# Kernel optimization log

Hardware: AMD Instinct MI355X
Metric: run time of the kernel (lower is better)

The kernel has to match this reference:

```python
import jax, jax.numpy as jnp
import numpy as np

NB_ATOMS = 128
NB_CH = 1
ATOM = 12          # atom_size
BATCH = 8
HW = 75            # -> 64x64 patch grid
LAM = 0.1          # soft-threshold level of the L1 proximal
UNROLL = 2         # unroll_steps
FISTA_ITERS = 15   # fixed inner FISTA iterations (replaces res-based stop)


def _prox(u):
    # soft-thresholding (prox of lam*||.||_1)
    return jnp.sign(u) * jnp.maximum(jnp.abs(u) - LAM, 0.0)


def _conv(x, w):
    # valid cross-correlation, NCHW / OIHW (== F.conv2d)
    return jax.lax.conv_general_dilated(x, w, (1, 1), 'VALID',
                                        dimension_numbers=('NCHW', 'OIHW', 'NCHW'))


def _fold(patches, H, W):
    # patches: [B, Ph, Pw, a, a] -> overlap-add to [B, 1, H, W] (== F.fold)
    B, Ph, Pw, a, _ = patches.shape
    out = jnp.zeros((B, H, W), patches.dtype)
    for di in range(a):              # fixed small kernel loop (a*a = 144 slots)
        for dj in range(a):
            out = out.at[:, di:di + Ph, dj:dj + Pw].add(patches[:, :, :, di, dj])
    return out[:, None]


def _fista(c0, X, q, mu):
    # standard FISTA on 0.5*||D^T c - y_patch||^2 + lam*||c||_1 with step mu
    def body(i, st):
        c, z, t = st
        cn = _prox(z - (z @ X - q) * mu)
        tn = (1.0 + jnp.sqrt(1.0 + 4.0 * t * t)) / 2.0
        zn = cn + ((t - 1.0) / tn) * (cn - c)
        return (cn, zn, tn)
    c, _, _ = jax.lax.fori_loop(0, FISTA_ITERS, body, (c0, c0, jnp.float32(1.0)))
    return c


def setup_inputs() -> dict:
    key = jax.random.key(0)
    k1, k2 = jax.random.split(key)
    y = jax.random.normal(k1, (BATCH, NB_CH, HW, HW), dtype=jnp.float32)
    atoms = jax.random.normal(k2, (NB_ATOMS, NB_CH, ATOM, ATOM), dtype=jnp.float32) / 1500.0
    beta = jnp.float32(0.1)
    mu = jnp.float32(1.0)
    return {"y": y, "atoms": atoms, "beta": beta, "mu": mu}


def reference(y, atoms, beta, mu):
    B, C, H, W = y.shape
    N, a = atoms.shape[0], atoms.shape[-1]
    beta = jax.nn.relu(beta)
    mu = jax.nn.relu(mu)
    # normalize atoms: zero-mean, unit L2 rows, then spectral norm / sqrt(mu)
    A = atoms - atoms.mean(axis=(1, 2, 3), keepdims=True)
    Af = A.reshape(N, -1)
    Af = Af / jnp.linalg.norm(Af, axis=1, keepdims=True)
    Af = Af / (jnp.linalg.norm(Af, ord=2) * jnp.sqrt(mu))
    atoms_n = Af.reshape(N, C, a, a)
    X = Af @ Af.T                                   # [N, N] gram
    Ph, Pw = H - a + 1, W - a + 1
    n_patch = B * Ph * Pw
    mean_filter = jnp.ones((1, 1, a, a), y.dtype) / (a * a)
    patch_mean = _conv(y, mean_filter).reshape(n_patch, 1, 1, 1)
    divisors = _fold(jnp.ones((B, Ph, Pw, a, a), y.dtype), H, W)  # overlap counts
    goal = y
    c = jnp.zeros((n_patch, N), y.dtype)
    sg = jax.lax.stop_gradient
    for _ in range(UNROLL):
        q = _conv(goal, atoms_n).transpose(0, 2, 3, 1).reshape(n_patch, N)
        cf = sg(_fista(sg(c), sg(X), sg(q), sg(mu)))   # torch.no_grad inner solve
        cf = _prox(cf - (cf @ X - q) * mu)             # one differentiable step
        pred = jnp.einsum('pn,ncij->pcij', cf, atoms_n) + patch_mean  # [P,1,a,a]
        pred = _fold(pred.reshape(B, Ph, Pw, a, a), H, W)
        goal = (y + beta * pred) / (1.0 + beta * divisors)
        c = cf
    return goal
```

## Files before the change

kernel.cpp:

```cpp
#include <hip/hip_runtime.h>
#include <stdint.h>

#define AA 144
#define LAM 0.1f

#define OFS_SC    0
#define OFS_AF1   64
#define OFS_G     36928
#define OFS_S0    53312
#define OFS_S1    69696
#define OFS_X     86080
#define OFS_PM    139328
#define OFS_GOAL  172096
#define OFS_CF    4411456
#define OFS_PRED  8605760
#define OFS_ATB   OFS_S0
#define OFS_ANTB  OFS_S1


typedef __attribute__((ext_vector_type(8))) short short8_t;
typedef __attribute__((ext_vector_type(4))) float f32x4;
typedef __attribute__((ext_vector_type(2))) float f32x2;

__device__ __forceinline__ unsigned short f2bf(float f) {
    union { float f; uint32_t u; } x; x.f = f;
    uint32_t u = x.u;
    return (unsigned short)((u + 0x7FFFu + ((u >> 16) & 1u)) >> 16);
}
__device__ __forceinline__ float bf2f(unsigned short u) {
    union { float f; uint32_t i; } x; x.i = ((uint32_t)u) << 16; return x.f;
}
__device__ __forceinline__ uint32_t pack_bf(float a, float b) {
    union { float f; uint32_t u; } xa, xb; xa.f = a; xb.f = b;
    return __builtin_amdgcn_perm(xb.u + 0x8000u, xa.u + 0x8000u, 0x07060302u);
}

#define PSTR 136
__global__ __launch_bounds__(1024) void k_setup(const float* atoms, const float* mu_p,
                                                float* ws, const float* y) {
    __shared__ unsigned short ABf[128 * 168];
    __shared__ unsigned short Pb[2][128 * PSTR];
    __shared__ float tr_arr[10];
    __shared__ float v[128];
    __shared__ float red[256];
    int t = threadIdx.x;
    if (blockIdx.x != 0) {
        int e = (blockIdx.x - 1) * 1024 + t;
        if (e < 45000) ws[OFS_GOAL + e] = y[e];
        if (e < 32768) {
            int b = e >> 12, pi = (e >> 6) & 63, pj = e & 63;
            const float* yb = y + b * 5625;
            float s = 0.f;
            for (int di = 0; di < 12; ++di) {
                const float* row = yb + (pi + di) * 75 + pj;
                #pragma unroll
                for (int dj = 0; dj < 12; ++dj) s += row[dj];
            }
            ws[OFS_PM + e] = s * (1.0f / 144.0f);
        }
        return;
    }
    int lane = t & 63, w = t >> 6;
    int col = lane & 15, quad = lane >> 4;
    if (t < 10) tr_arr[t] = (t == 0) ? 128.0f : 0.f;

    {
        int a = t >> 3, sub = t & 7;
        const float* ap = atoms + a * AA + sub * 18;
        float s = 0.f;
        #pragma unroll
        for (int k = 0; k < 18; ++k) s += ap[k];
        s += __shfl_xor(s, 1, 8); s += __shfl_xor(s, 2, 8); s += __shfl_xor(s, 4, 8);
        float mean = s * (1.0f / 144.0f);
        float ss = 0.f;
        #pragma unroll
        for (int k = 0; k < 18; ++k) { float d = ap[k] - mean; ss = fmaf(d, d, ss); }
        ss += __shfl_xor(ss, 1, 8); ss += __shfl_xor(ss, 2, 8); ss += __shfl_xor(ss, 4, 8);
        float rn = 1.0f / sqrtf(ss);
        #pragma unroll
        for (int k = 0; k < 18; ++k) {
            float av = (ap[k] - mean) * rn;
            ws[OFS_AF1 + a * AA + sub * 18 + k] = av;
            ABf[a * 168 + sub * 18 + k] = f2bf(av);
        }
        if (sub == 0) {
            #pragma unroll
            for (int k = AA; k < 160; ++k) ABf[a * 168 + k] = 0;
        }
    }
    __syncthreads();

    {
        uint32_t* D32 = (uint32_t*)Pb[0];
        float* G = ws + OFS_G;
        int mt = w & 7, gh = w >> 3;
        short8_t af[5];
        #pragma unroll
        for (int s = 0; s < 5; ++s)
            af[s] = *(const short8_t*)&ABf[(mt * 16 + col) * 168 + s * 32 + quad * 8];
        #pragma unroll
        for (int gi = 0; gi < 2; ++gi) {
            int g = gh * 2 + gi;
            short8_t b0[5], b1[5];
            #pragma unroll
            for (int s = 0; s < 5; ++s) {
                b0[s] = *(const short8_t*)&ABf[((2 * g) * 16 + col) * 168 + s * 32 + quad * 8];
                b1[s] = *(const short8_t*)&ABf[((2 * g + 1) * 16 + col) * 168 + s * 32 + quad * 8];
            }
            f32x4 a0 = (f32x4){0.f, 0.f, 0.f, 0.f};
            f32x4 a1 = (f32x4){0.f, 0.f, 0.f, 0.f};
            #pragma unroll
            for (int s = 0; s < 5; ++s) {
                a0 = __builtin_amdgcn_mfma_f32_16x16x32_bf16(af[s], b0[s], a0, 0, 0, 0);
                a1 = __builtin_amdgcn_mfma_f32_16x16x32_bf16(af[s], b1[s], a1, 0, 0, 0);
            }
            #pragma unroll
            for (int r = 0; r < 4; ++r) {
                int m = mt * 16 + quad * 4 + r;
                G[m * 128 + g * 32 + col] = a0[r];
                G[m * 128 + g * 32 + 16 + col] = a1[r];
                D32[m * 68 + g * 16 + col] = pack_bf(a0[r], a1[r]);
            }
        }
    }
    __syncthreads();

    int cur = 0;
    #pragma unroll 1
    for (int j = 0; j < 8; ++j) {
        float trn = tr_arr[j];
        float inv2 = 1.0f / (trn * trn);
        const unsigned short* S = Pb[cur];
        uint32_t* D32 = (uint32_t*)Pb[cur ^ 1];
        int mt = w & 7, nh = w >> 3;
        short8_t af[4];
        #pragma unroll
        for (int s = 0; s < 4; ++s)
            af[s] = *(const short8_t*)&S[(mt * 16 + col) * PSTR + s * 32 + quad * 8];
        #pragma unroll
        for (int pr = 0; pr < 2; ++pr) {
            int ntE = 4 * nh + 2 * pr, ntO = ntE + 1;
            short8_t bE[4], bO[4];
            #pragma unroll
            for (int s = 0; s < 4; ++s) {
                bE[s] = *(const short8_t*)&S[(ntE * 16 + col) * PSTR + s * 32 + quad * 8];
                bO[s] = *(const short8_t*)&S[(ntO * 16 + col) * PSTR + s * 32 + quad * 8];
            }
            f32x4 aE = (f32x4){0.f, 0.f, 0.f, 0.f};
            f32x4 aO = (f32x4){0.f, 0.f, 0.f, 0.f};
            #pragma unroll
            for (int s = 0; s < 4; ++s) {
                aE = __builtin_amdgcn_mfma_f32_16x16x32_bf16(af[s], bE[s], aE, 0, 0, 0);
                aO = __builtin_amdgcn_mfma_f32_16x16x32_bf16(af[s], bO[s], aO, 0, 0, 0);
            }
            int nE = ntE * 16 + col, nO = ntO * 16 + col;
            #pragma unroll
            for (int r = 0; r < 4; ++r) {
                float x0 = aE[r] * inv2, x1 = aO[r] * inv2;
                int row = mt * 16 + quad * 4 + r;
                D32[row * 68 + (ntE >> 1) * 16 + col] = pack_bf(x0, x1);
                if (row == nE) atomicAdd(&tr_arr[j + 1], x0);
                if (row == nO) atomicAdd(&tr_arr[j + 1], x1);
            }
        }
        __syncthreads();
        cur ^= 1;
    }

    {
        int a = t >> 3, sub = t & 7;
        const unsigned short* S = Pb[cur];
        float s = 0.f;
        #pragma unroll
        for (int k = 0; k < 16; ++k) s += bf2f(S[a * PSTR + sub * 16 + k]);
        s += __shfl_xor(s, 1, 8); s += __shfl_xor(s, 2, 8); s += __shfl_xor(s, 4, 8);
        if (sub == 0) v[a] = s;
    }
    __syncthreads();
    {
        int a = t >> 3, sub = t & 7;
        const float* G = ws + OFS_G;
        float wv = 0.f;
        #pragma unroll
        for (int k = 0; k < 16; ++k)
            wv = fmaf(G[a * 128 + sub * 16 + k], v[sub * 16 + k], wv);
        wv += __shfl_xor(wv, 1, 8); wv += __shfl_xor(wv, 2, 8); wv += __shfl_xor(wv, 4, 8);
        if (sub == 0) { red[a] = v[a] * wv; red[128 + a] = v[a] * v[a]; }
    }
    __syncthreads();
    for (int off = 64; off > 0; off >>= 1) {
        if (t < off) { red[t] += red[t + off]; red[128 + t] += red[128 + t + off]; }
        __syncthreads();
    }
    if (t == 0) {
        float lam = red[0] / red[128];
        float mu = fmaxf(mu_p[0], 0.0f);
        ws[OFS_SC + 16] = 1.0f / (lam * mu);
        ws[OFS_SC + 17] = 1.0f / (sqrtf(lam) * sqrtf(mu));
    }
}

__global__ __launch_bounds__(256) void k_finalize(float* ws) {
    int idx = blockIdx.x * 256 + threadIdx.x;
    float scX = ws[OFS_SC + 16], scA = ws[OFS_SC + 17];
    if (idx < 16384) {
        int n = idx >> 7, ks = idx & 127;
        int g = ks >> 5, rem = ks & 31, u = rem >> 1, v = rem & 1;
        int k = g * 32 + v * 16 + u;
        ((unsigned short*)(ws + OFS_X))[idx] = f2bf(ws[OFS_G + n * 128 + k] * scX);
    } else if (idx < 36864) {
        int e = idx - 16384;
        int n = e / 160, k = e - n * 160;
        float v = (k < 144) ? ws[OFS_AF1 + n * 144 + k] * scA : 0.f;
        ((unsigned short*)(ws + OFS_ATB))[e] = f2bf(v);
    } else {
        int e = idx - 36864;
        int jp = e >> 7, ks = e & 127;
        int g = ks >> 5, rem = ks & 31, u = rem >> 1, v = rem & 1;
        int n = g * 32 + v * 16 + u;
        ((unsigned short*)(ws + OFS_ANTB))[e] = f2bf(ws[OFS_AF1 + n * 144 + jp] * scA);
    }
}

__global__ __launch_bounds__(256) void k_fista(const unsigned short* XPB, const float* goal,
                                               const unsigned short* ATB,
                                               const unsigned short* ANTBP,
                                               const float* pm, float* cfg, float* pred,
                                               const float* mu_p, int first, int write_cf) {
    __shared__ float gls[12 * 44];
    __shared__ unsigned short Atile[32 * 168];
    __shared__ unsigned short Zbuf[2][32 * 136];
    int t = threadIdx.x;
    int lane = t & 63, w = t >> 6;
    int col = lane & 15, quad = lane >> 4;
    int nb = w * 32;
    int blk = blockIdx.x;
    int b = blk >> 7, pi = (blk >> 1) & 63, h = blk & 1;
    int p0 = blk * 32;
    float mu = fmaxf(mu_p[0], 0.0f);
    const f32x2 mu2 = (f32x2){mu, mu};
    const f32x2 lam2 = (f32x2){LAM, LAM};
    const f32x2 nlam2 = (f32x2){-LAM, -LAM};

    for (int e = t; e < 528; e += 256) {
        int r = e / 44, cc = e - r * 44;
        int gc = h * 32 + cc;
        gls[e] = (gc < 75) ? goal[b * 5625 + (pi + r) * 75 + gc] : 0.f;
    }
    __syncthreads();
    {
        uint32_t* A32 = (uint32_t*)Atile;
        #pragma unroll
        for (int i = 0; i < 10; ++i) {
            int pe = t + i * 256;
            int m = pe / 80, q32 = pe - m * 80;
            int kk = q32 * 2;
            float v0 = 0.f, v1 = 0.f;
            if (kk < 144) {
                int di = kk / 12, dj = kk - di * 12;
                v0 = gls[di * 44 + m + dj];
                int k1 = kk + 1, di1 = k1 / 12, dj1 = k1 - di1 * 12;
                v1 = gls[di1 * 44 + m + dj1];
            }
            A32[m * 84 + q32] = pack_bf(v0, v1);
        }
    }
    __syncthreads();

    f32x2 qv2[2][4];
    {
        short8_t bfq[2][5];
        #pragma unroll
        for (int nt = 0; nt < 2; ++nt)
            #pragma unroll
            for (int s = 0; s < 5; ++s)
                bfq[nt][s] = *(const short8_t*)&ATB[(nb + nt * 16 + col) * 160 + s * 32 + quad * 8];
        #pragma unroll
        for (int mt = 0; mt < 2; ++mt) {
            short8_t af[5];
            #pragma unroll
            for (int s = 0; s < 5; ++s)
                af[s] = *(const short8_t*)&Atile[(mt * 16 + col) * 168 + s * 32 + quad * 8];
            f32x4 acc0 = (f32x4){0.f, 0.f, 0.f, 0.f};
            f32x4 acc1 = (f32x4){0.f, 0.f, 0.f, 0.f};
            #pragma unroll
            for (int s = 0; s < 5; ++s) {
                acc0 = __builtin_amdgcn_mfma_f32_16x16x32_bf16(af[s], bfq[0][s], acc0, 0, 0, 0);
                acc1 = __builtin_amdgcn_mfma_f32_16x16x32_bf16(af[s], bfq[1][s], acc1, 0, 0, 0);
            }
            #pragma unroll
            for (int r = 0; r < 4; ++r) qv2[mt][r] = (f32x2){acc0[r], acc1[r]};
        }
    }

    short8_t xf[2][4];
    #pragma unroll
    for (int nt = 0; nt < 2; ++nt)
        #pragma unroll
        for (int s = 0; s < 4; ++s)
            xf[nt][s] = *(const short8_t*)&XPB[(nb + nt * 16 + col) * 128 + s * 32 + quad * 8];

    uint32_t* Z32w = (uint32_t*)Zbuf[0];
    f32x2 cv2[2][4], zo2[2][4];
    #pragma unroll
    for (int mt = 0; mt < 2; ++mt)
        #pragma unroll
        for (int r = 0; r < 4; ++r) {
            int row = mt * 16 + quad * 4 + r;
            int p = p0 + row;
            float c0 = 0.f, c1 = 0.f;
            if (!first) {
                c0 = cfg[p * 128 + nb + col];
                c1 = cfg[p * 128 + nb + 16 + col];
            }
            cv2[mt][r] = (f32x2){c0, c1};
            zo2[mt][r] = (f32x2){c0, c1};
            Z32w[row * 68 + 16 * w + col] = pack_bf(c0, c1);
        }
    __syncthreads();

    f32x4 acc[2][2];
    auto matmul = [&](const unsigned short* Zr) {
        short8_t af[2][4];
        #pragma unroll
        for (int mt = 0; mt < 2; ++mt)
            #pragma unroll
            for (int s = 0; s < 4; ++s)
                af[mt][s] = *(const short8_t*)&Zr[(mt * 16 + col) * 136 + s * 32 + quad * 8];
        #pragma unroll
        for (int mt = 0; mt < 2; ++mt)
            #pragma unroll
            for (int nt = 0; nt < 2; ++nt)
                acc[mt][nt] = (f32x4){0.f, 0.f, 0.f, 0.f};
        #pragma unroll
        for (int s = 0; s < 4; ++s)
            #pragma unroll
            for (int mt = 0; mt < 2; ++mt)
                #pragma unroll
                for (int nt = 0; nt < 2; ++nt)
                    acc[mt][nt] = __builtin_amdgcn_mfma_f32_16x16x32_bf16(
                        af[mt][s], xf[nt][s], acc[mt][nt], 0, 0, 0);
    };

    float tm = 1.0f;
    int cur = 0;
    #pragma unroll 1
    for (int it = 0; it < 14; ++it) {
        matmul(Zbuf[cur]);
        float tnn = 0.5f * (1.0f + sqrtf(1.0f + 4.0f * tm * tm));
        float fm = (tm - 1.0f) / tnn;
        tm = tnn;
        f32x2 fm2 = (f32x2){fm, fm};
        uint32_t* Zw = (uint32_t*)Zbuf[cur ^ 1];
        #pragma unroll
        for (int mt = 0; mt < 2; ++mt)
            #pragma unroll
            for (int r = 0; r < 4; ++r) {
                f32x2 a2 = (f32x2){acc[mt][0][r], acc[mt][1][r]};
                f32x2 u2 = mu2 * (qv2[mt][r] - a2) + zo2[mt][r];
                f32x2 cl2 = __builtin_elementwise_min(
                                __builtin_elementwise_max(u2, nlam2), lam2);
                f32x2 cn2 = u2 - cl2;
                f32x2 zn2 = fm2 * (cn2 - cv2[mt][r]) + cn2;
                cv2[mt][r] = cn2;
                zo2[mt][r] = zn2;
                Zw[(mt * 16 + quad * 4 + r) * 68 + 16 * w + col] = pack_bf(zn2[0], zn2[1]);
            }
        __syncthreads();
        cur ^= 1;
    }
    {
        matmul(Zbuf[cur]);
        uint32_t* Zw = (uint32_t*)Zbuf[cur ^ 1];
        #pragma unroll
        for (int mt = 0; mt < 2; ++mt)
            #pragma unroll
            for (int r = 0; r < 4; ++r) {
                f32x2 a2 = (f32x2){acc[mt][0][r], acc[mt][1][r]};
                f32x2 u2 = mu2 * (qv2[mt][r] - a2) + zo2[mt][r];
                f32x2 cl2 = __builtin_elementwise_min(
                                __builtin_elementwise_max(u2, nlam2), lam2);
                f32x2 cn2 = u2 - cl2;
                cv2[mt][r] = cn2;
                Zw[(mt * 16 + quad * 4 + r) * 68 + 16 * w + col] = pack_bf(cn2[0], cn2[1]);
            }
        __syncthreads();
        cur ^= 1;
    }
    {
        matmul(Zbuf[cur]);
        uint32_t* Zw = (uint32_t*)Zbuf[cur ^ 1];
        #pragma unroll
        for (int mt = 0; mt < 2; ++mt)
            #pragma unroll
            for (int r = 0; r < 4; ++r) {
                int row = mt * 16 + quad * 4 + r;
                f32x2 a2 = (f32x2){acc[mt][0][r], acc[mt][1][r]};
                f32x2 u2 = mu2 * (qv2[mt][r] - a2) + cv2[mt][r];
                f32x2 cl2 = __builtin_elementwise_min(
                                __builtin_elementwise_max(u2, nlam2), lam2);
                f32x2 cf2 = u2 - cl2;
                if (write_cf) {
                    cfg[(p0 + row) * 128 + nb + col] = cf2[0];
                    cfg[(p0 + row) * 128 + nb + 16 + col] = cf2[1];
                }
                Zw[row * 68 + 16 * w + col] = pack_bf(cf2[0], cf2[1]);
            }
        __syncthreads();
        cur ^= 1;
    }

    {
        int jt0 = (w == 0) ? 0 : (2 * w + 1);
        int jtn = (w == 0) ? 3 : 2;
        const unsigned short* Zr = Zbuf[cur];
        short8_t af[2][4];
        #pragma unroll
        for (int mt = 0; mt < 2; ++mt)
            #pragma unroll
            for (int s = 0; s < 4; ++s)
                af[mt][s] = *(const short8_t*)&Zr[(mt * 16 + col) * 136 + s * 32 + quad * 8];
        f32x4 accp[2][3];
        #pragma unroll
        for (int mt = 0; mt < 2; ++mt)
            #pragma unroll
            for (int ji = 0; ji < 3; ++ji)
                accp[mt][ji] = (f32x4){0.f, 0.f, 0.f, 0.f};
        #pragma unroll
        for (int ji = 0; ji < 3; ++ji) {
            if (ji < jtn) {
                int jt = jt0 + ji;
                short8_t bf4[4];
                #pragma unroll
                for (int s = 0; s < 4; ++s)
                    bf4[s] = *(const short8_t*)&ANTBP[(jt * 16 + col) * 128 + s * 32 + quad * 8];
                #pragma unroll
                for (int mt = 0; mt < 2; ++mt)
                    #pragma unroll
                    for (int s = 0; s < 4; ++s)
                        accp[mt][ji] = __builtin_amdgcn_mfma_f32_16x16x32_bf16(
                            af[mt][s], bf4[s], accp[mt][ji], 0, 0, 0);
            }
        }
        #pragma unroll
        for (int mt = 0; mt < 2; ++mt)
            #pragma unroll
            for (int r = 0; r < 4; ++r) {
                int p = p0 + mt * 16 + quad * 4 + r;
                float pmv = pm[p];
                #pragma unroll
                for (int ji = 0; ji < 3; ++ji)
                    if (ji < jtn)
                        pred[p * 144 + (jt0 + ji) * 16 + col] = accp[mt][ji][r] + pmv;
            }
    }
}

__global__ __launch_bounds__(256) void k_fold(const float* y, const float* beta_p,
                                              const float* pred, float* goal,
                                              float* out, int write_out) {
    __shared__ float P[12 * 832];
    int i = blockIdx.x, b = blockIdx.y;
    int t = threadIdx.x;
    for (int di = 0; di < 12; ++di) {
        int pi = i - di;
        if ((unsigned)pi >= 64u) continue;
        int base = (b << 12) + (pi << 6);
        #pragma unroll
        for (int it = 0; it < 3; ++it) {
            int e = t + it * 256;
            int pj = e / 12, dj = e - pj * 12;
            P[di * 832 + pj * 13 + dj] = pred[(base + pj) * AA + di * 12 + dj];
        }
    }
    __syncthreads();
    if (t >= 75) return;
    int j = t;
    float S = 0.f;
    for (int di = 0; di < 12; ++di) {
        if ((unsigned)(i - di) >= 64u) continue;
        const float* Pd = &P[di * 832];
        #pragma unroll
        for (int dj = 0; dj < 12; ++dj) {
            int pj = j - dj;
            if ((unsigned)pj >= 64u) continue;
            S += Pd[pj * 13 + dj];
        }
    }
    int ci = min(i, 11) - max(i - 63, 0) + 1;
    int cj = min(j, 11) - max(j - 63, 0) + 1;
    float beta = fmaxf(beta_p[0], 0.0f);
    int idx = i * 75 + j;
    float yv = y[b * 5625 + idx];
    float g = (yv + beta * S) / (1.0f + beta * (float)(ci * cj));
    if (write_out) out[b * 5625 + idx] = g;
    else           goal[b * 5625 + idx] = g;
}

extern "C" void kernel_launch(void* const* d_in, const int* in_sizes, int n_in,
                              void* d_out, int out_size, void* d_ws, size_t ws_size,
                              hipStream_t stream) {
    const float* y     = (const float*)d_in[0];
    const float* atoms = (const float*)d_in[1];
    const float* beta  = (const float*)d_in[2];
    const float* mu    = (const float*)d_in[3];
    float* out = (float*)d_out;
    float* ws = (float*)d_ws;

    k_setup<<<46, 1024, 0, stream>>>(atoms, mu, ws, y);
    k_finalize<<<216, 256, 0, stream>>>(ws);

    for (int u = 0; u < 2; ++u) {
        k_fista<<<1024, 256, 0, stream>>>((const unsigned short*)(ws + OFS_X),
                                          ws + OFS_GOAL,
                                          (const unsigned short*)(ws + OFS_ATB),
                                          (const unsigned short*)(ws + OFS_ANTB),
                                          ws + OFS_PM, ws + OFS_CF, ws + OFS_PRED,
                                          mu, u == 0 ? 1 : 0, u == 0 ? 1 : 0);
        k_fold<<<dim3(75, 8), 256, 0, stream>>>(y, beta, ws + OFS_PRED,
                                                ws + OFS_GOAL, out, u == 1 ? 1 : 0);
    }
}
```

Before: 214.1 us.

## Store FISTA coefficients and patch predictions as bf16, read goal directly

The intermediate coefficient buffer is now stored as packed bf16 pairs instead of fp32, and the per-patch prediction buffer is written as bf16 with round-half-up conversion and widened back to fp32 in the fold kernel. The goal tile staging through shared memory and its barrier are removed, so the input patch matrix is built by reading goal straight from global memory. The aim is to roughly halve the global traffic of the large intermediate buffers, at the cost of extra rounding in the stored predictions and coefficients, and less coalesced, repeated global reads for the patch build.

```diff
diff --git a/kernel.cpp b/kernel.cpp
--- a/kernel.cpp
+++ b/kernel.cpp
@@ -26,6 +26,10 @@
     union { float f; uint32_t u; } x; x.f = f;
     uint32_t u = x.u;
     return (unsigned short)((u + 0x7FFFu + ((u >> 16) & 1u)) >> 16);
+}
+__device__ __forceinline__ unsigned short f2bh(float f) {
+    union { float f; uint32_t u; } x; x.f = f;
+    return (unsigned short)((x.u + 0x8000u) >> 16);
 }
 __device__ __forceinline__ float bf2f(unsigned short u) {
     union { float f; uint32_t i; } x; x.i = ((uint32_t)u) << 16; return x.f;
@@ -225,9 +229,9 @@
 __global__ __launch_bounds__(256) void k_fista(const unsigned short* XPB, const float* goal,
                                                const unsigned short* ATB,
                                                const unsigned short* ANTBP,
-                                               const float* pm, float* cfg, float* pred,
+                                               const float* pm, uint32_t* cfgb,
+                                               unsigned short* predh,
                                                const float* mu_p, int first, int write_cf) {
-    __shared__ float gls[12 * 44];
     __shared__ unsigned short Atile[32 * 168];
     __shared__ unsigned short Zbuf[2][32 * 136];
     int t = threadIdx.x;
@@ -242,13 +246,8 @@
     const f32x2 lam2 = (f32x2){LAM, LAM};
     const f32x2 nlam2 = (f32x2){-LAM, -LAM};
 
-    for (int e = t; e < 528; e += 256) {
-        int r = e / 44, cc = e - r * 44;
-        int gc = h * 32 + cc;
-        gls[e] = (gc < 75) ? goal[b * 5625 + (pi + r) * 75 + gc] : 0.f;
-    }
-    __syncthreads();
-    {
+    {
+        const float* gb = goal + b * 5625 + pi * 75 + h * 32;
         uint32_t* A32 = (uint32_t*)Atile;
         #pragma unroll
         for (int i = 0; i < 10; ++i) {
@@ -258,9 +257,9 @@
             float v0 = 0.f, v1 = 0.f;
             if (kk < 144) {
                 int di = kk / 12, dj = kk - di * 12;
-                v0 = gls[di * 44 + m + dj];
+                v0 = gb[di * 75 + m + dj];
                 int k1 = kk + 1, di1 = k1 / 12, dj1 = k1 - di1 * 12;
-                v1 = gls[di1 * 44 + m + dj1];
+                v1 = gb[di1 * 75 + m + dj1];
             }
             A32[m * 84 + q32] = pack_bf(v0, v1);
         }
@@ -307,15 +306,16 @@
         #pragma unroll
         for (int r = 0; r < 4; ++r) {
             int row = mt * 16 + quad * 4 + r;
-            int p = p0 + row;
+            uint32_t pk = 0u;
             float c0 = 0.f, c1 = 0.f;
             if (!first) {
-                c0 = cfg[p * 128 + nb + col];
-                c1 = cfg[p * 128 + nb + 16 + col];
+                pk = cfgb[(p0 + row) * 64 + 16 * w + col];
+                c0 = bf2f((unsigned short)(pk & 0xFFFFu));
+                c1 = bf2f((unsigned short)(pk >> 16));
             }
             cv2[mt][r] = (f32x2){c0, c1};
             zo2[mt][r] = (f32x2){c0, c1};
-            Z32w[row * 68 + 16 * w + col] = pack_bf(c0, c1);
+            Z32w[row * 68 + 16 * w + col] = pk;
         }
     __syncthreads();
 
@@ -400,11 +400,9 @@
                 f32x2 cl2 = __builtin_elementwise_min(
                                 __builtin_elementwise_max(u2, nlam2), lam2);
                 f32x2 cf2 = u2 - cl2;
-                if (write_cf) {
-                    cfg[(p0 + row) * 128 + nb + col] = cf2[0];
-                    cfg[(p0 + row) * 128 + nb + 16 + col] = cf2[1];
-                }
-                Zw[row * 68 + 16 * w + col] = pack_bf(cf2[0], cf2[1]);
+                uint32_t pk = pack_bf(cf2[0], cf2[1]);
+                if (write_cf) cfgb[(p0 + row) * 64 + 16 * w + col] = pk;
+                Zw[row * 68 + 16 * w + col] = pk;
             }
         __syncthreads();
         cur ^= 1;
@@ -451,13 +449,13 @@
                 #pragma unroll
                 for (int ji = 0; ji < 3; ++ji)
                     if (ji < jtn)
-                        pred[p * 144 + (jt0 + ji) * 16 + col] = accp[mt][ji][r] + pmv;
+                        predh[p * 144 + (jt0 + ji) * 16 + col] = f2bh(accp[mt][ji][r] + pmv);
             }
     }
 }
 
 __global__ __launch_bounds__(256) void k_fold(const float* y, const float* beta_p,
-                                              const float* pred, float* goal,
+                                              const unsigned short* predh, float* goal,
                                               float* out, int write_out) {
     __shared__ float P[12 * 832];
     int i = blockIdx.x, b = blockIdx.y;
@@ -470,7 +468,7 @@
         for (int it = 0; it < 3; ++it) {
             int e = t + it * 256;
             int pj = e / 12, dj = e - pj * 12;
-            P[di * 832 + pj * 13 + dj] = pred[(base + pj) * AA + di * 12 + dj];
+            P[di * 832 + pj * 13 + dj] = bf2f(predh[(base + pj) * AA + di * 12 + dj]);
         }
     }
     __syncthreads();
@@ -515,9 +513,11 @@
                                           ws + OFS_GOAL,
                                           (const unsigned short*)(ws + OFS_ATB),
                                           (const unsigned short*)(ws + OFS_ANTB),
-                                          ws + OFS_PM, ws + OFS_CF, ws + OFS_PRED,
+                                          ws + OFS_PM, (uint32_t*)(ws + OFS_CF),
+                                          (unsigned short*)(ws + OFS_PRED),
                                           mu, u == 0 ? 1 : 0, u == 0 ? 1 : 0);
-        k_fold<<<dim3(75, 8), 256, 0, stream>>>(y, beta, ws + OFS_PRED,
+        k_fold<<<dim3(75, 8), 256, 0, stream>>>(y, beta,
+                                                (const unsigned short*)(ws + OFS_PRED),
                                                 ws + OFS_GOAL, out, u == 1 ? 1 : 0);
     }
 }
```

After: 212.7 us, median of 2. No clear change (-0.6%).
